# Performance work log

Measured on AMD Instinct MI355X. Metric: run time of the kernel, lower is better.

The kernel has to match this reference:

```python
import jax, jax.numpy as jnp
import numpy as np

BUCKET_SIZE = 64
N_HASHES = 8
SELF_MASK_VAL = -1e5
EPS = 1e-6


def look_one_back(x):
    # concat each block with the previous block (wrap-around), along block-inner axis
    prev = jnp.roll(x, 1, axis=1)
    return jnp.concatenate([x, prev], axis=2)


def setup_inputs() -> dict:
    key = jax.random.key(0)
    k1, k2, k3 = jax.random.split(key, 3)
    B, S, D = 8, 4096, 64
    n_buckets = S // BUCKET_SIZE  # 64
    qk = jax.random.normal(k1, (B, S, D), dtype=jnp.float32)
    v = jax.random.normal(k2, (B, S, D), dtype=jnp.float32)
    rotations = jax.random.normal(k3, (1, D, N_HASHES, n_buckets // 2), dtype=jnp.float32)
    return {"qk": qk, "v": v, "rotations": rotations}


def reference(qk, v, rotations):
    B, S, D = qk.shape
    n_buckets = S // BUCKET_SIZE
    n_bins = n_buckets

    # --- hash_vectors ---
    rot = jnp.broadcast_to(rotations, (B, D, N_HASHES, n_buckets // 2))
    rotated = jnp.einsum('btf,bfhi->bhti', qk, rot)            # [B,H,S,nb/2]
    rotated = jnp.concatenate([rotated, -rotated], axis=-1)    # [B,H,S,nb]
    buckets = jnp.argmax(rotated, axis=-1)                     # [B,H,S]
    offsets = (jnp.arange(N_HASHES) * n_buckets)[None, :, None]
    buckets = (buckets + offsets).reshape(B, N_HASHES * S)     # [B,H*S]

    # --- sort tokens by (bucket, position) ---
    ticker = jnp.arange(N_HASHES * S)[None, :]
    buckets_and_t = S * buckets + (ticker % S)
    sticker = jnp.argsort(buckets_and_t, axis=-1)              # stable sort
    undo_sort = jnp.argsort(sticker, axis=-1)
    st = sticker % S                                           # original positions

    sqk = jnp.take_along_axis(qk, st[..., None], axis=1)       # [B,H*S,D]
    sv = jnp.take_along_axis(v, st[..., None], axis=1)

    n_blocks = N_HASHES * n_bins
    bq_t = st.reshape(B, n_blocks, -1)                         # [B,nb,bs]
    bqk = sqk.reshape(B, n_blocks, -1, D)
    bv = sv.reshape(B, n_blocks, -1, D)

    bq = bqk
    # make_unit_length
    bk = bqk * jax.lax.rsqrt(jnp.sum(bqk * bqk, axis=-1, keepdims=True) + EPS)
    bk = look_one_back(bk)                                     # [B,nb,2bs,D]
    bv = look_one_back(bv)
    bkv_t = look_one_back(bq_t[..., None])[..., 0]             # [B,nb,2bs]

    dots = jnp.einsum('bhie,bhje->bhij', bq, bk) * (D ** -0.5)  # [B,nb,bs,2bs]

    # self-mask (as written in source: keep dots where positions equal, -1e5 elsewhere)
    self_mask = bq_t[:, :, :, None] == bkv_t[:, :, None, :]
    dots = jnp.where(self_mask, dots, SELF_MASK_VAL)

    dots_lse = jax.scipy.special.logsumexp(dots, axis=-1, keepdims=True)
    probs = jnp.exp(dots - dots_lse)
    bo = jnp.einsum('buij,buje->buie', probs, bv)              # [B,nb,bs,D]

    so = bo.reshape(B, N_HASHES * S, D)
    slogits = dots_lse.reshape(B, N_HASHES * S)

    # unsort
    o = jnp.take_along_axis(so, undo_sort[..., None], axis=1)
    logits = jnp.take_along_axis(slogits, undo_sort, axis=1)

    # combine over hash rounds
    o = o.reshape(B, N_HASHES, S, D)
    logits = logits.reshape(B, N_HASHES, S, 1)
    w = jnp.exp(logits - jax.scipy.special.logsumexp(logits, axis=1, keepdims=True))
    out = jnp.sum(o * w, axis=1)                               # [B,S,D]
    return out, buckets
```

## Files before the change

kernel.cpp:

```cpp
#include <hip/hip_runtime.h>

#define BB 8
#define SS 4096
#define DD 64
#define NH 8
#define NBKT 64
#define OUT_V_ELEMS (BB*SS*DD)

__global__ __launch_bounds__(256) void lsh_hash_kernel(
    const float* __restrict__ qk,
    const float* __restrict__ v,
    const float* __restrict__ rot,
    float* __restrict__ out)
{
    __shared__ float qk_s[64 * 64];

    const int tid = threadIdx.x;
    const int blk = blockIdx.x;
    const int b   = blk >> 7;
    const int r   = blk & 127;
    const int hq  = r >> 6;
    const int tc  = r & 63;
    const int t0  = tc * 64;

    {
        const float4* v4 = (const float4*)v;
        float4*       o4 = (float4*)out;
        const int base = blk * 512 + tid;
        o4[base]       = v4[base];
        o4[base + 256] = v4[base + 256];
    }

    {
        const float4* qg = (const float4*)qk;
#pragma unroll
        for (int k = 0; k < 4; ++k) {
            const int p   = tid + k * 256;
            const int tok = p >> 4, g = p & 15;
            const float4 x = qg[(b * SS + t0 + tok) * 16 + g];
            *(float4*)&qk_s[tok * 64 + ((g ^ (tok & 15)) << 2)] = x;
        }
    }
    __syncthreads();

    const int lane = tid & 63;
    const int h    = hq * 4 + (tid >> 6);
    const int h_u  = __builtin_amdgcn_readfirstlane(h);
    const float* __restrict__ rot_h = rot + h_u * 32;

    float acc[32];
#pragma unroll
    for (int i = 0; i < 32; ++i) acc[i] = 0.0f;

    const int lrow = lane * 64;
    const int lsw  = lane & 15;

#pragma unroll
    for (int fg = 0; fg < 16; ++fg) {
        const float4 q4 = *(const float4*)&qk_s[lrow + ((fg ^ lsw) << 2)];
        const float qa[4] = {q4.x, q4.y, q4.z, q4.w};
#pragma unroll
        for (int j = 0; j < 4; ++j) {
            const float* __restrict__ rp = rot_h + (fg * 4 + j) * (NH * 32);
            float rr[32];
#pragma unroll
            for (int i = 0; i < 32; ++i) rr[i] = rp[i];
            const float qf = qa[j];
#pragma unroll
            for (int i = 0; i < 32; ++i)
                acc[i] = fmaf(qf, rr[i], acc[i]);
        }
    }

    float pv = acc[0]; int pi = 0;
    float nv = -acc[0]; int ni = 0;
#pragma unroll
    for (int i = 1; i < 32; ++i) {
        if (acc[i]  > pv) { pv = acc[i];  pi = i; }
        if (-acc[i] > nv) { nv = -acc[i]; ni = i; }
    }
    const int idx = (pv >= nv) ? pi : (ni + 32);
    out[OUT_V_ELEMS + b * (NH * SS) + h * SS + t0 + lane] = (float)(idx + h * NBKT);
}

extern "C" void kernel_launch(void* const* d_in, const int* in_sizes, int n_in,
                              void* d_out, int out_size, void* d_ws, size_t ws_size,
                              hipStream_t stream) {
    const float* qk  = (const float*)d_in[0];
    const float* v   = (const float*)d_in[1];
    const float* rot = (const float*)d_in[2];
    float* out = (float*)d_out;
    hipLaunchKernelGGL(lsh_hash_kernel, dim3(1024), dim3(256), 0, stream,
                       qk, v, rot, out);
}
```

Baseline: 26.29 us.

## Register-tile the hash projection with LDS-staged rotations and double-buffered q loads

Restructures the hash projection as a register-blocked outer product. Each thread now accumulates 8 tokens × 16 rotation columns, and the rotation slice is staged once per block in swizzled LDS instead of being read from global memory per wave. Query fragments are double-buffered across feature groups. The argmax is split across lane pairs and merged with xor shuffles, using an index tie-break that keeps first-max semantics. The grid shrinks to 512 blocks of 128 threads, so occupancy drops and register pressure rises (128 accumulators plus 64 query registers) in exchange for more reuse per LDS read.

```diff
diff --git a/kernel.cpp b/kernel.cpp
--- a/kernel.cpp
+++ b/kernel.cpp
@@ -7,80 +7,133 @@
 #define NBKT 64
 #define OUT_V_ELEMS (BB*SS*DD)
 
-__global__ __launch_bounds__(256) void lsh_hash_kernel(
+__global__ __launch_bounds__(128) void lsh_hash_kernel(
     const float* __restrict__ qk,
     const float* __restrict__ v,
     const float* __restrict__ rot,
     float* __restrict__ out)
 {
-    __shared__ float qk_s[64 * 64];
+    __shared__ float q_s[128 * 64];
+    __shared__ float rot_s[64 * 128];
 
     const int tid = threadIdx.x;
     const int blk = blockIdx.x;
-    const int b   = blk >> 7;
-    const int r   = blk & 127;
-    const int hq  = r >> 6;
-    const int tc  = r & 63;
-    const int t0  = tc * 64;
+    const int b   = blk >> 6;
+    const int hq  = (blk >> 5) & 1;
+    const int ch  = blk & 31;
+    const int t0  = ch * 128;
 
     {
         const float4* v4 = (const float4*)v;
         float4*       o4 = (float4*)out;
-        const int base = blk * 512 + tid;
-        o4[base]       = v4[base];
-        o4[base + 256] = v4[base + 256];
+        const int base = blk * 1024 + tid;
+#pragma unroll
+        for (int j = 0; j < 8; ++j)
+            o4[base + j * 128] = v4[base + j * 128];
     }
 
     {
         const float4* qg = (const float4*)qk;
 #pragma unroll
-        for (int k = 0; k < 4; ++k) {
-            const int p   = tid + k * 256;
-            const int tok = p >> 4, g = p & 15;
-            const float4 x = qg[(b * SS + t0 + tok) * 16 + g];
-            *(float4*)&qk_s[tok * 64 + ((g ^ (tok & 15)) << 2)] = x;
+        for (int k = 0; k < 16; ++k) {
+            const int p   = k * 128 + tid;
+            const int tok = p >> 4, fc = p & 15;
+            const float4 x = qg[(b * SS + t0 + tok) * 16 + fc];
+            *(float4*)&q_s[tok * 64 + ((fc ^ ((tok >> 3) & 7)) << 2)] = x;
+        }
+    }
+    {
+        const float4* rg = (const float4*)rot;
+#pragma unroll
+        for (int k = 0; k < 16; ++k) {
+            const int p = k * 128 + tid;
+            const int f = p >> 5, c = p & 31;
+            const float4 x = rg[f * 64 + hq * 32 + c];
+            const int slot = (c & 3) * 8 + (c >> 2);
+            *(float4*)&rot_s[f * 128 + slot * 4] = x;
         }
     }
     __syncthreads();
 
     const int lane = tid & 63;
-    const int h    = hq * 4 + (tid >> 6);
-    const int h_u  = __builtin_amdgcn_readfirstlane(h);
-    const float* __restrict__ rot_h = rot + h_u * 32;
+    const int wv   = tid >> 6;
+    const int tx   = lane & 7;
+    const int ty   = lane >> 3;
+    const int trow = (wv * 64 + tx * 8) * 64;
+    const int rbase = ty * 4;
 
-    float acc[32];
+    float acc[8][16];
 #pragma unroll
-    for (int i = 0; i < 32; ++i) acc[i] = 0.0f;
+    for (int a = 0; a < 8; ++a)
+#pragma unroll
+        for (int c = 0; c < 16; ++c) acc[a][c] = 0.0f;
 
-    const int lrow = lane * 64;
-    const int lsw  = lane & 15;
+    float4 qA[8], qB[8];
+#define LOADQ(dst, fq_)                                                    \
+    {                                                                      \
+        const int qc = (((fq_) ^ tx) << 2);                                \
+        _Pragma("unroll")                                                  \
+        for (int a = 0; a < 8; ++a)                                        \
+            dst[a] = *(const float4*)&q_s[trow + a * 64 + qc];             \
+    }
+#define COMPUTE(qr, fq_)                                                   \
+    {                                                                      \
+        _Pragma("unroll")                                                  \
+        for (int df = 0; df < 4; ++df) {                                   \
+            const int f = (fq_) * 4 + df;                                  \
+            float4 r4[4];                                                  \
+            _Pragma("unroll")                                              \
+            for (int p = 0; p < 4; ++p)                                    \
+                r4[p] = *(const float4*)&rot_s[f * 128 + p * 32 + rbase];  \
+            const float rr[16] = {r4[0].x, r4[0].y, r4[0].z, r4[0].w,      \
+                                  r4[1].x, r4[1].y, r4[1].z, r4[1].w,      \
+                                  r4[2].x, r4[2].y, r4[2].z, r4[2].w,      \
+                                  r4[3].x, r4[3].y, r4[3].z, r4[3].w};     \
+            _Pragma("unroll")                                              \
+            for (int a = 0; a < 8; ++a) {                                  \
+                const float qf = df == 0 ? qr[a].x : df == 1 ? qr[a].y     \
+                                 : df == 2 ? qr[a].z : qr[a].w;            \
+                _Pragma("unroll")                                          \
+                for (int c = 0; c < 16; ++c)                               \
+                    acc[a][c] = fmaf(qf, rr[c], acc[a][c]);                \
+            }                                                              \
+        }                                                                  \
+    }
+
+    LOADQ(qA, 0);
+#pragma unroll 1
+    for (int fq = 0; fq < 16; fq += 2) {
+        LOADQ(qB, fq + 1);
+        COMPUTE(qA, fq);
+        if (fq + 2 < 16) LOADQ(qA, fq + 2);
+        COMPUTE(qB, fq + 1);
+    }
+
+    const int h     = hq * 4 + (ty >> 1);
+    const int dbase = (ty & 1) * 16;
+    float* bout = out + OUT_V_ELEMS + b * (NH * SS) + h * SS + t0 + wv * 64 + tx * 8;
 
 #pragma unroll
-    for (int fg = 0; fg < 16; ++fg) {
-        const float4 q4 = *(const float4*)&qk_s[lrow + ((fg ^ lsw) << 2)];
-        const float qa[4] = {q4.x, q4.y, q4.z, q4.w};
+    for (int a = 0; a < 8; ++a) {
+        float pv = acc[a][0]; int pi = dbase;
+        float nv = -acc[a][0]; int ni = dbase;
 #pragma unroll
-        for (int j = 0; j < 4; ++j) {
-            const float* __restrict__ rp = rot_h + (fg * 4 + j) * (NH * 32);
-            float rr[32];
-#pragma unroll
-            for (int i = 0; i < 32; ++i) rr[i] = rp[i];
-            const float qf = qa[j];
-#pragma unroll
-            for (int i = 0; i < 32; ++i)
-                acc[i] = fmaf(qf, rr[i], acc[i]);
+        for (int c = 1; c < 16; ++c) {
+            const float x = acc[a][c];
+            if (x  > pv) { pv = x;  pi = dbase + c; }
+            if (-x > nv) { nv = -x; ni = dbase + c; }
         }
+        const float opv = __shfl_xor(pv, 8);
+        const int   opi = __shfl_xor(pi, 8);
+        const float onv = __shfl_xor(nv, 8);
+        const int   oni = __shfl_xor(ni, 8);
+        if (opv > pv || (opv == pv && opi < pi)) { pv = opv; pi = opi; }
+        if (onv > nv || (onv == nv && oni < ni)) { nv = onv; ni = oni; }
+        const int idx = (pv >= nv) ? pi : (ni + 32);
+        if ((ty & 1) == 0) bout[a] = (float)(idx + h * NBKT);
     }
-
-    float pv = acc[0]; int pi = 0;
-    float nv = -acc[0]; int ni = 0;
-#pragma unroll
-    for (int i = 1; i < 32; ++i) {
-        if (acc[i]  > pv) { pv = acc[i];  pi = i; }
-        if (-acc[i] > nv) { nv = -acc[i]; ni = i; }
-    }
-    const int idx = (pv >= nv) ? pi : (ni + 32);
-    out[OUT_V_ELEMS + b * (NH * SS) + h * SS + t0 + lane] = (float)(idx + h * NBKT);
+#undef LOADQ
+#undef COMPUTE
 }
 
 extern "C" void kernel_launch(void* const* d_in, const int* in_sizes, int n_in,
@@ -90,6 +143,6 @@
     const float* v   = (const float*)d_in[1];
     const float* rot = (const float*)d_in[2];
     float* out = (float*)d_out;
-    hipLaunchKernelGGL(lsh_hash_kernel, dim3(1024), dim3(256), 0, stream,
+    hipLaunchKernelGGL(lsh_hash_kernel, dim3(512), dim3(128), 0, stream,
                        qk, v, rot, out);
 }
```

Measured after the change: 25.20 us. 4.2% less time.

## Compute LSH hash projections with split-bf16 MFMA and repair near-tie argmaxes

Applied to the files above, without the earlier changes.

Replaces the scalar FP32 rotation matmul with bf16x3 (hi/lo split) MFMA 16x16x32 on matrix cores. A pre-kernel splits the rotations into hi/lo bf16 once per call. The main kernel now handles all 8 hashes per 64-token tile and flags tokens whose top-two margin is small. A repair kernel recomputes flagged tokens in exact FP32 so the argmax matches the reference. This adds two extra launches, more LDS per block and a correctness dependence on the tie threshold.

```diff
diff --git a/kernel.cpp b/kernel.cpp
--- a/kernel.cpp
+++ b/kernel.cpp
@@ -1,86 +1,213 @@
 #include <hip/hip_runtime.h>
 
-#define BB 8
 #define SS 4096
-#define DD 64
-#define NH 8
-#define NBKT 64
-#define OUT_V_ELEMS (BB*SS*DD)
-
-__global__ __launch_bounds__(256) void lsh_hash_kernel(
-    const float* __restrict__ qk,
-    const float* __restrict__ v,
-    const float* __restrict__ rot,
-    float* __restrict__ out)
-{
-    __shared__ float qk_s[64 * 64];
+#define OUT_V (8*4096*64)
+#define ROT_LO_OFS 32768
+#define FLAGS_OFS  65536
+#define EPS 0.02f
+
+typedef short bf16x8 __attribute__((ext_vector_type(8)));
+typedef float f32x4  __attribute__((ext_vector_type(4)));
+
+__device__ __forceinline__ unsigned short f2bf(float x) {
+    unsigned int u = __float_as_uint(x);
+    u = u + 0x7FFFu + ((u >> 16) & 1u);
+    return (unsigned short)(u >> 16);
+}
+
+__global__ __launch_bounds__(256) void lsh_pre(const float* __restrict__ rot,
+                                               unsigned short* __restrict__ wh,
+                                               unsigned short* __restrict__ wl) {
+    const int idx = blockIdx.x * 256 + threadIdx.x;
+    const int d = idx >> 6, f = idx & 63;
+    const float x = rot[f * 256 + d];
+    const unsigned short hi = f2bf(x);
+    const float hif = __uint_as_float((unsigned int)hi << 16);
+    wh[d * 64 + f] = hi;
+    wl[d * 64 + f] = f2bf(x - hif);
+}
+
+__global__ __launch_bounds__(256, 2) void lsh_main(const float* __restrict__ qk,
+                                                   const float* __restrict__ v,
+                                                   float* __restrict__ out,
+                                                   const unsigned short* __restrict__ wh,
+                                                   const unsigned short* __restrict__ wl,
+                                                   unsigned char* __restrict__ flags) {
+    __shared__ __align__(16) unsigned short qh[64 * 64];
+    __shared__ __align__(16) unsigned short ql[64 * 64];
+    __shared__ __align__(16) unsigned short rh[256 * 64];
+    __shared__ __align__(16) unsigned short rl[256 * 64];
 
     const int tid = threadIdx.x;
     const int blk = blockIdx.x;
-    const int b   = blk >> 7;
-    const int r   = blk & 127;
-    const int hq  = r >> 6;
-    const int tc  = r & 63;
-    const int t0  = tc * 64;
+    const int b   = blk >> 6;
+    const int t0  = (blk & 63) * 64;
 
     {
         const float4* v4 = (const float4*)v;
         float4*       o4 = (float4*)out;
-        const int base = blk * 512 + tid;
-        o4[base]       = v4[base];
-        o4[base + 256] = v4[base + 256];
+        const int base = blk * 1024 + tid;
+#pragma unroll
+        for (int j = 0; j < 4; ++j) o4[base + j * 256] = v4[base + j * 256];
     }
 
     {
-        const float4* qg = (const float4*)qk;
+        const float4* qg = (const float4*)(qk + (size_t)(b * SS + t0) * 64);
 #pragma unroll
         for (int k = 0; k < 4; ++k) {
-            const int p   = tid + k * 256;
-            const int tok = p >> 4, g = p & 15;
-            const float4 x = qg[(b * SS + t0 + tok) * 16 + g];
-            *(float4*)&qk_s[tok * 64 + ((g ^ (tok & 15)) << 2)] = x;
+            const int p = k * 256 + tid;
+            const int tok = p >> 4, fg = p & 15;
+            const float4 x = qg[p];
+            const float xs[4] = {x.x, x.y, x.z, x.w};
+            unsigned int hp[2], lp[2];
+            unsigned short hv[4], lv[4];
+#pragma unroll
+            for (int e = 0; e < 4; ++e) {
+                hv[e] = f2bf(xs[e]);
+                lv[e] = f2bf(xs[e] - __uint_as_float((unsigned int)hv[e] << 16));
+            }
+            hp[0] = hv[0] | ((unsigned int)hv[1] << 16);
+            hp[1] = hv[2] | ((unsigned int)hv[3] << 16);
+            lp[0] = lv[0] | ((unsigned int)lv[1] << 16);
+            lp[1] = lv[2] | ((unsigned int)lv[3] << 16);
+            const int chunkp = (fg >> 1) ^ (tok & 7);
+            const int ub = tok * 64 + chunkp * 8 + (fg & 1) * 4;
+            *(uint2*)&qh[ub] = make_uint2(hp[0], hp[1]);
+            *(uint2*)&ql[ub] = make_uint2(lp[0], lp[1]);
+        }
+    }
+    {
+        const uint4* rhg = (const uint4*)wh;
+        const uint4* rlg = (const uint4*)wl;
+#pragma unroll
+        for (int k = 0; k < 8; ++k) {
+            const int p = k * 256 + tid;
+            const int row = p >> 3, c = p & 7;
+            const int cp = c ^ (row & 7);
+            *(uint4*)&rh[row * 64 + cp * 8] = rhg[p];
+            *(uint4*)&rl[row * 64 + cp * 8] = rlg[p];
         }
     }
     __syncthreads();
 
     const int lane = tid & 63;
-    const int h    = hq * 4 + (tid >> 6);
-    const int h_u  = __builtin_amdgcn_readfirstlane(h);
-    const float* __restrict__ rot_h = rot + h_u * 32;
-
-    float acc[32];
-#pragma unroll
-    for (int i = 0; i < 32; ++i) acc[i] = 0.0f;
-
-    const int lrow = lane * 64;
-    const int lsw  = lane & 15;
-
-#pragma unroll
-    for (int fg = 0; fg < 16; ++fg) {
-        const float4 q4 = *(const float4*)&qk_s[lrow + ((fg ^ lsw) << 2)];
-        const float qa[4] = {q4.x, q4.y, q4.z, q4.w};
-#pragma unroll
-        for (int j = 0; j < 4; ++j) {
-            const float* __restrict__ rp = rot_h + (fg * 4 + j) * (NH * 32);
-            float rr[32];
-#pragma unroll
-            for (int i = 0; i < 32; ++i) rr[i] = rp[i];
-            const float qf = qa[j];
-#pragma unroll
-            for (int i = 0; i < 32; ++i)
-                acc[i] = fmaf(qf, rr[i], acc[i]);
-        }
-    }
-
-    float pv = acc[0]; int pi = 0;
-    float nv = -acc[0]; int ni = 0;
-#pragma unroll
-    for (int i = 1; i < 32; ++i) {
-        if (acc[i]  > pv) { pv = acc[i];  pi = i; }
-        if (-acc[i] > nv) { nv = -acc[i]; ni = i; }
-    }
-    const int idx = (pv >= nv) ? pi : (ni + 32);
-    out[OUT_V_ELEMS + b * (NH * SS) + h * SS + t0 + lane] = (float)(idx + h * NBKT);
+    const int w    = tid >> 6;
+    const int l15  = lane & 15;
+    const int g    = lane >> 4;
+
+    f32x4 acc[4][4];
+#pragma unroll
+    for (int dt = 0; dt < 4; ++dt)
+#pragma unroll
+        for (int nt = 0; nt < 4; ++nt) acc[dt][nt] = (f32x4){0.f, 0.f, 0.f, 0.f};
+
+#pragma unroll
+    for (int nt = 0; nt < 4; ++nt) {
+        const int brow = nt * 16 + l15;
+        bf16x8 Bh[2], Bl[2];
+#pragma unroll
+        for (int ks = 0; ks < 2; ++ks) {
+            const int idx = brow * 64 + ((ks * 4 + g) ^ (brow & 7)) * 8;
+            Bh[ks] = *(const bf16x8*)&qh[idx];
+            Bl[ks] = *(const bf16x8*)&ql[idx];
+        }
+#pragma unroll
+        for (int dt = 0; dt < 4; ++dt) {
+            const int arow = (w * 4 + dt) * 16 + l15;
+            bf16x8 Ah[2], Al[2];
+#pragma unroll
+            for (int ks = 0; ks < 2; ++ks) {
+                const int idx = arow * 64 + ((ks * 4 + g) ^ (arow & 7)) * 8;
+                Ah[ks] = *(const bf16x8*)&rh[idx];
+                Al[ks] = *(const bf16x8*)&rl[idx];
+            }
+            f32x4 c = acc[dt][nt];
+#pragma unroll
+            for (int ks = 0; ks < 2; ++ks) {
+                c = __builtin_amdgcn_mfma_f32_16x16x32_bf16(Al[ks], Bh[ks], c, 0, 0, 0);
+                c = __builtin_amdgcn_mfma_f32_16x16x32_bf16(Ah[ks], Bl[ks], c, 0, 0, 0);
+                c = __builtin_amdgcn_mfma_f32_16x16x32_bf16(Ah[ks], Bh[ks], c, 0, 0, 0);
+            }
+            acc[dt][nt] = c;
+        }
+    }
+
+#define UPD(vv, ii) {                                                     \
+        if ((vv) > m1)      { m2 = m1; m1 = (vv); i1 = (ii); }            \
+        else if ((vv) == m1){ m2 = m1; if ((ii) < i1) i1 = (ii); }        \
+        else if ((vv) > m2) { m2 = (vv); }                                \
+    }
+#pragma unroll
+    for (int hh = 0; hh < 2; ++hh) {
+        const int h = 2 * w + hh;
+#pragma unroll
+        for (int nt = 0; nt < 4; ++nt) {
+            float m1 = -1e30f, m2 = -1e30f;
+            int i1 = 0;
+#pragma unroll
+            for (int dtl = 0; dtl < 2; ++dtl) {
+                const int dt = hh * 2 + dtl;
+#pragma unroll
+                for (int r = 0; r < 4; ++r) {
+                    const float vv = acc[dt][nt][r];
+                    const int dl = dtl * 16 + g * 4 + r;
+                    UPD(vv, dl);
+                    UPD(-vv, 32 + dl);
+                }
+            }
+#pragma unroll
+            for (int m = 16; m <= 32; m <<= 1) {
+                const float om1 = __shfl_xor(m1, m);
+                const int   oi1 = __shfl_xor(i1, m);
+                const float om2 = __shfl_xor(m2, m);
+                UPD(om1, oi1);
+                m2 = fmaxf(m2, om2);
+            }
+            if (g == 0) {
+                const int t = t0 + nt * 16 + l15;
+                const int oidx = (b * 8 + h) * SS + t;
+                out[OUT_V + oidx] = (float)(i1 + h * 64);
+                flags[oidx] = (m1 - m2 < EPS) ? 1 : 0;
+            }
+        }
+    }
+#undef UPD
+}
+
+__global__ __launch_bounds__(256) void lsh_repair(const float* __restrict__ qk,
+                                                  const float* __restrict__ rot,
+                                                  float* __restrict__ out,
+                                                  const unsigned char* __restrict__ flags) {
+    const int lane = threadIdx.x & 63;
+    const int wid  = (blockIdx.x * 256 + threadIdx.x) >> 6;
+#pragma unroll 1
+    for (int gi = 0; gi < 2; ++gi) {
+        const int base = wid * 128 + gi * 64;
+        unsigned long long mask = __ballot(flags[base + lane] != 0);
+        while (mask) {
+            const int bit = __ffsll((unsigned long long)mask) - 1;
+            mask &= mask - 1;
+            const int pair = base + bit;
+            const int t  = pair & 4095;
+            const int bh = pair >> 12;
+            const int h  = bh & 7;
+            const float* qrow = qk + (size_t)((bh >> 3) * SS + t) * 64;
+            const int col = h * 32 + (lane & 31);
+            float acc = 0.f;
+#pragma unroll
+            for (int f = 0; f < 64; ++f)
+                acc = fmaf(qrow[f], rot[f * 256 + col], acc);
+            float val = (lane < 32) ? acc : -acc;
+            int   idx = lane;
+#pragma unroll
+            for (int m = 1; m <= 32; m <<= 1) {
+                const float ov = __shfl_xor(val, m);
+                const int   oi = __shfl_xor(idx, m);
+                if (ov > val || (ov == val && oi < idx)) { val = ov; idx = oi; }
+            }
+            if (lane == 0) out[OUT_V + pair] = (float)(idx + h * 64);
+        }
+    }
 }
 
 extern "C" void kernel_launch(void* const* d_in, const int* in_sizes, int n_in,
@@ -90,6 +217,11 @@
     const float* v   = (const float*)d_in[1];
     const float* rot = (const float*)d_in[2];
     float* out = (float*)d_out;
-    hipLaunchKernelGGL(lsh_hash_kernel, dim3(1024), dim3(256), 0, stream,
-                       qk, v, rot, out);
-}
+    unsigned short* wh    = (unsigned short*)d_ws;
+    unsigned short* wl    = (unsigned short*)((char*)d_ws + ROT_LO_OFS);
+    unsigned char*  flags = (unsigned char*)((char*)d_ws + FLAGS_OFS);
+
+    hipLaunchKernelGGL(lsh_pre,    dim3(64),  dim3(256), 0, stream, rot, wh, wl);
+    hipLaunchKernelGGL(lsh_main,   dim3(512), dim3(256), 0, stream, qk, v, out, wh, wl, flags);
+    hipLaunchKernelGGL(lsh_repair, dim3(512), dim3(256), 0, stream, qk, rot, out, flags);
+}
```

Result: slower. 33.96 us (+29.2%).
